# Performance work log

Measured on AMD Instinct MI355X. Metric: run time of the kernel, lower is better.

The kernel has to match this reference:

```python
import jax, jax.numpy as jnp
import numpy as np

B, D, C = 8192, 2048, 1000

def setup_inputs() -> dict:
    key = jax.random.key(0)
    k1, k2, k3 = jax.random.split(key, 3)
    x = jax.random.normal(k1, (B, D), dtype=jnp.float32)
    W = jax.random.normal(k2, (D, C), dtype=jnp.float32) * (1.0 / np.sqrt(D))
    b = jax.random.normal(k3, (C,), dtype=jnp.float32) * 0.01
    return {"x": x, "W": W, "b": b}

def reference(x, W, b):
    # inner classifier: logits out[b, c]
    out = jnp.dot(x, W) + b  # [B, C]
    # leave-one-out logsumexp per class, fused:
    # lse_k = logsumexp(out[:, != k]) = lse_all + log1p(-exp(out_k - lse_all))
    lse = jax.nn.logsumexp(out, axis=1, keepdims=True)  # [B, 1]
    loo = lse + jnp.log1p(-jnp.exp(out - lse))           # [B, C]
    # c_out = -loo; return c_out + out
    return out - loo
```

## Files before the change

### kernel.cpp

```cpp
#include <hip/hip_runtime.h>
#include <hip/hip_bf16.h>
#include <math.h>

#define BDIM 8192
#define DDIM 2048
#define CDIM 1000
#define NPAD 1024
#define BK   64

#define WS_BT_OFFSET  33554432ULL
#define WS_P0_OFFSET  37748736ULL
#define WS_P1_OFFSET  54132736ULL
#define WS_NEED       70516736ULL

typedef __attribute__((ext_vector_type(8))) short short8;
typedef __attribute__((ext_vector_type(4))) float floatx4;

__device__ __forceinline__ unsigned short f2bf(float f) {
    union { float f; unsigned u; } a; a.f = f;
    unsigned u = a.u;
    u = (u + 0x7fff + ((u >> 16) & 1)) >> 16;
    return (unsigned short)u;
}

__device__ __forceinline__ float bf2f(unsigned short h) {
    union { unsigned u; float f; } a; a.u = ((unsigned)h) << 16;
    return a.f;
}

__device__ __forceinline__ void async_copy16(const void* gp, void* lp) {
    __builtin_amdgcn_global_load_lds(
        (const __attribute__((address_space(1))) void*)gp,
        (__attribute__((address_space(3))) void*)lp,
        16, 0, 0);
}

__global__ __launch_bounds__(256) void cvt_kernel(
    const float* __restrict__ x, unsigned short* __restrict__ xb,
    const float* __restrict__ W, unsigned short* __restrict__ Bt)
{
    const int blk = blockIdx.x;
    const int t   = threadIdx.x;
    if (blk < 16384) {
        int i = blk * 256 + t;
        float4 v = ((const float4*)x)[i];
        ushort4 o;
        o.x = f2bf(v.x); o.y = f2bf(v.y); o.z = f2bf(v.z); o.w = f2bf(v.w);
        ((ushort4*)xb)[i] = o;
    } else {
        __shared__ float tile[32][33];
        const int b2 = blk - 16384;
        const int k0 = (b2 & 63) * 32;
        const int n0 = (b2 >> 6) * 32;
        const int tx = t & 31, ty = t >> 5;
        #pragma unroll
        for (int i = 0; i < 4; i++) {
            int k = k0 + ty + i * 8;
            int n = n0 + tx;
            tile[ty + i * 8][tx] = (n < CDIM) ? W[(size_t)k * CDIM + n] : 0.0f;
        }
        __syncthreads();
        #pragma unroll
        for (int i = 0; i < 4; i++) {
            int n = n0 + ty + i * 8;
            int k = k0 + tx;
            Bt[(size_t)n * DDIM + k] = f2bf(tile[tx][ty + i * 8]);
        }
    }
}

template <bool BF16OUT>
__device__ __forceinline__ void gemm_body(
    const unsigned short* __restrict__ A,
    const unsigned short* __restrict__ Bt,
    void* __restrict__ Cv,
    int mBase, int nBase, int kBase, int kIters,
    unsigned short* As, unsigned short* Bs)
{
    const int t    = threadIdx.x;
    const int wave = t >> 6;
    const int lane = t & 63;
    const int wm   = wave & 1;
    const int wn   = wave >> 1;
    const int quad = lane >> 4;
    const int l16  = lane & 15;

    floatx4 acc[4][4] = {};

    const int rowA = t >> 3;
    const int csw  = ((t & 7) ^ (rowA & 7)) * 16;
    const char* Ag = (const char*)A  + ((size_t)(mBase + rowA) * DDIM + kBase) * 2 + csw;
    const char* Bg = (const char*)Bt + ((size_t)(nBase + rowA) * DDIM + kBase) * 2 + csw;
    char* AsDst = (char*)As + t * 16;
    char* BsDst = (char*)Bs + t * 16;

    const int xorb0 = ((0 * 4 + quad) ^ (l16 & 7)) * 8;
    const int xorb1 = ((1 * 4 + quad) ^ (l16 & 7)) * 8;

    for (int kt = 0; kt < kIters * BK; kt += BK) {
        const char* a = Ag + kt * 2;
        const char* b = Bg + kt * 2;
        #pragma unroll
        for (int r = 0; r < 4; r++) {
            async_copy16(a + (size_t)r * 32 * DDIM * 2, AsDst + r * 4096);
            async_copy16(b + (size_t)r * 32 * DDIM * 2, BsDst + r * 4096);
        }
        __syncthreads();

        #pragma unroll
        for (int ks = 0; ks < 2; ks++) {
            const int xorb = ks ? xorb1 : xorb0;
            short8 af[4], bfr[4];
            #pragma unroll
            for (int mi = 0; mi < 4; mi++)
                af[mi] = *(const short8*)(As + (wm * 64 + mi * 16 + l16) * BK + xorb);
            #pragma unroll
            for (int ni = 0; ni < 4; ni++)
                bfr[ni] = *(const short8*)(Bs + (wn * 64 + ni * 16 + l16) * BK + xorb);
            #pragma unroll
            for (int mi = 0; mi < 4; mi++)
                #pragma unroll
                for (int ni = 0; ni < 4; ni++)
                    acc[mi][ni] = __builtin_amdgcn_mfma_f32_16x16x32_bf16(
                        af[mi], bfr[ni], acc[mi][ni], 0, 0, 0);
        }
        __syncthreads();
    }

    #pragma unroll
    for (int mi = 0; mi < 4; mi++) {
        int row0 = mBase + wm * 64 + mi * 16 + quad * 4;
        #pragma unroll
        for (int ni = 0; ni < 4; ni++) {
            int col = nBase + wn * 64 + ni * 16 + l16;
            if (col < CDIM) {
                #pragma unroll
                for (int rg = 0; rg < 4; rg++) {
                    if (BF16OUT)
                        ((unsigned short*)Cv)[(size_t)(row0 + rg) * CDIM + col] =
                            f2bf(acc[mi][ni][rg]);
                    else
                        ((float*)Cv)[(size_t)(row0 + rg) * CDIM + col] = acc[mi][ni][rg];
                }
            }
        }
    }
}

__global__ __launch_bounds__(256, 2) void gemm_single_kernel(
    const unsigned short* __restrict__ A,
    const unsigned short* __restrict__ Bt,
    float* __restrict__ C0)
{
    __shared__ unsigned short As[128 * BK];
    __shared__ unsigned short Bs[128 * BK];

    const int L   = blockIdx.x;
    const int xcd = L & 7;
    const int s   = L >> 3;
    const int m_t = xcd * 8 + (s >> 3);
    const int n_t = s & 7;

    gemm_body<false>(A, Bt, C0, m_t * 128, n_t * 128, 0, DDIM / BK, As, Bs);
}


#define HBUF (256 * BK)

#define STAGE_A2(BASE, EXT, KO)                                               \
    do {                                                                      \
        _Pragma("unroll")                                                     \
        for (int h = 0; h < 2; h++) {                                         \
            const int row_ = rA0 + (EXT) + h * 128;                           \
            async_copy16(gA + (size_t)row_ * DDIM + (KO),                     \
                         (BASE) + row_ * BK + c8);                            \
        }                                                                     \
    } while (0)

#define STAGE_B2(BASE, EXT, KO)                                               \
    do {                                                                      \
        _Pragma("unroll")                                                     \
        for (int h = 0; h < 2; h++) {                                         \
            const int row_ = rB0 + (EXT) + h * 128;                           \
            async_copy16(gB + (size_t)row_ * DDIM + (KO),                     \
                         (BASE) + row_ * BK + c8);                            \
        }                                                                     \
    } while (0)

#define LOADA_(BASE, MQ)                                                      \
    do {                                                                      \
        _Pragma("unroll")                                                     \
        for (int mf = 0; mf < 4; mf++) {                                      \
            const int r_ = (arA + (MQ) * 64 + mf * 16) * BK;                  \
            af[mf][0] = *(const short8*)((BASE) + r_ + xorb0);                \
            af[mf][1] = *(const short8*)((BASE) + r_ + xorb1);                \
        }                                                                     \
    } while (0)

#define LOADB_(BASE, NQ, BF)                                                  \
    do {                                                                      \
        _Pragma("unroll")                                                     \
        for (int nf = 0; nf < 2; nf++) {                                      \
            const int r_ = (arB + (NQ) * 32 + nf * 16) * BK;                  \
            BF[nf][0] = *(const short8*)((BASE) + r_ + xorb0);                \
            BF[nf][1] = *(const short8*)((BASE) + r_ + xorb1);                \
        }                                                                     \
    } while (0)

#define MMAC(MQ, NQ, BF)                                                      \
    do {                                                                      \
        __builtin_amdgcn_s_setprio(1);                                        \
        _Pragma("unroll")                                                     \
        for (int mf = 0; mf < 4; mf++) {                                      \
            _Pragma("unroll")                                                 \
            for (int nf = 0; nf < 2; nf++) {                                  \
                floatx4 c_ = acc[(MQ) * 4 + mf][(NQ) * 2 + nf];               \
                c_ = __builtin_amdgcn_mfma_f32_16x16x32_bf16(                 \
                    af[mf][0], BF[nf][0], c_, 0, 0, 0);                       \
                c_ = __builtin_amdgcn_mfma_f32_16x16x32_bf16(                 \
                    af[mf][1], BF[nf][1], c_, 0, 0, 0);                       \
                acc[(MQ) * 4 + mf][(NQ) * 2 + nf] = c_;                       \
            }                                                                 \
        }                                                                     \
        __builtin_amdgcn_s_setprio(0);                                        \
    } while (0)

#define RAW_BARRIER() asm volatile("s_barrier" ::: "memory")
#define WAIT_VM(N)    asm volatile("s_waitcnt vmcnt(" #N ")" ::: "memory")
#define WAIT_LGKM0()  asm volatile("s_waitcnt lgkmcnt(0)" ::: "memory")

__global__ __launch_bounds__(512) void gemm8_kernel(
    const unsigned short* __restrict__ A,
    const unsigned short* __restrict__ Bt,
    unsigned short* __restrict__ P0, unsigned short* __restrict__ P1)
{
    __shared__ unsigned short As[2 * HBUF];
    __shared__ unsigned short Bs[2 * HBUF];

    const int t    = threadIdx.x;
    const int wave = t >> 6;
    const int lane = t & 63;
    const int wm   = wave >> 2;
    const int wn   = wave & 3;
    const int quad = lane >> 4;
    const int l16  = lane & 15;

    const int L    = blockIdx.x;
    const int g    = (L & 7) * 32 + (L >> 3);
    const int z    = g & 1;
    const int tid2 = g >> 1;
    const int mBase = (tid2 >> 2) * 256;
    const int nBase = (tid2 & 3) * 256;
    const int kBase = z * (DDIM / 2);
    const int NTt   = (DDIM / 2) / BK;

    const int c8  = (t & 7) << 3;
    const int q0  = t >> 3;
    const int csw = (((t & 7) ^ (q0 & 7)) << 3);
    const int rA0 = q0;
    const int rB0 = q0 + (q0 & 32);
    const unsigned short* gA = A  + (size_t)mBase * DDIM + kBase + csw;
    const unsigned short* gB = Bt + (size_t)nBase * DDIM + kBase + csw;

    const int xorb0 = ((0 * 4 + quad) ^ (l16 & 7)) << 3;
    const int xorb1 = ((1 * 4 + quad) ^ (l16 & 7)) << 3;
    const int arA = wm * 128 + l16;
    const int arB = wn * 64 + l16;

    floatx4 acc[8][4] = {};
    short8 af[4][2], bf0[2][2], bf1[2][2];

    STAGE_A2(As, 0, 0);
    STAGE_A2(As, 64, 0);
    STAGE_B2(Bs, 0, 0);
    STAGE_B2(Bs, 32, 0);
    STAGE_A2(As + HBUF, 0, BK);
    STAGE_A2(As + HBUF, 64, BK);
    STAGE_B2(Bs + HBUF, 0, BK);
    STAGE_B2(Bs + HBUF, 32, BK);
    WAIT_VM(8);
    RAW_BARRIER();
    LOADA_(As, 0);
    LOADB_(Bs, 0, bf0);
    WAIT_LGKM0();
    RAW_BARRIER();

    for (int j = 0; j < NTt; j++) {
        const int bo = (j & 1) * HBUF;
        unsigned short* const cA = (unsigned short*)As + bo;
        unsigned short* const cB = (unsigned short*)Bs + bo;
        const unsigned short* const nA = (const unsigned short*)As + (bo ^ HBUF);
        const unsigned short* const nB = (const unsigned short*)Bs + (bo ^ HBUF);
        const int  ko2 = (j + 2) * BK;
        const bool s2  = (j + 2 < NTt);

        if (s2) STAGE_A2(cA, 0, ko2);
        MMAC(0, 0, bf0);
        LOADB_(cB, 1, bf1);
        RAW_BARRIER();

        if (s2) STAGE_B2(cB, 0, ko2);
        MMAC(0, 1, bf1);
        LOADA_(cA, 1);
        RAW_BARRIER();

        if (s2) STAGE_B2(cB, 32, ko2);
        MMAC(1, 0, bf0);
        if (j < NTt - 2) WAIT_VM(6);
        else             WAIT_VM(0);
        RAW_BARRIER();

        if (s2) STAGE_A2(cA, 64, ko2);
        MMAC(1, 1, bf1);
        if (j + 1 < NTt) { LOADA_(nA, 0); LOADB_(nB, 0, bf0); }
        WAIT_LGKM0();
        RAW_BARRIER();
    }

    unsigned short* P = z ? P1 : P0;
    #pragma unroll
    for (int mfg = 0; mfg < 8; mfg++) {
        const int row0 = mBase + wm * 128 + mfg * 16 + quad * 4;
        #pragma unroll
        for (int nfg = 0; nfg < 4; nfg++) {
            const int col = nBase + wn * 64 + nfg * 16 + l16;
            if (col < CDIM) {
                #pragma unroll
                for (int rg = 0; rg < 4; rg++)
                    P[(size_t)(row0 + rg) * CDIM + col] = f2bf(acc[mfg][nfg][rg]);
            }
        }
    }
}

__global__ __launch_bounds__(256) void lse_kernel(
    float* __restrict__ out,
    const unsigned short* P0, const unsigned short* P1,
    const float* __restrict__ bias, int split)
{
    const int row = blockIdx.x;
    const int t   = threadIdx.x;
    __shared__ float red[8];

    const bool valid = t < (CDIM / 4);
    const int c0 = t * 4;

    float4 v = make_float4(-INFINITY, -INFINITY, -INFINITY, -INFINITY);
    float4 e = make_float4(0.f, 0.f, 0.f, 0.f);
    if (valid) {
        if (split) {
            ushort4 p0 = *(const ushort4*)(P0 + (size_t)row * CDIM + c0);
            ushort4 p1 = *(const ushort4*)(P1 + (size_t)row * CDIM + c0);
            v.x = bf2f(p0.x) + bf2f(p1.x);
            v.y = bf2f(p0.y) + bf2f(p1.y);
            v.z = bf2f(p0.z) + bf2f(p1.z);
            v.w = bf2f(p0.w) + bf2f(p1.w);
        } else {
            v = *(const float4*)(out + (size_t)row * CDIM + c0);
        }
        float4 bb = *(const float4*)(bias + c0);
        v.x += bb.x; v.y += bb.y; v.z += bb.z; v.w += bb.w;
    }

    float m = fmaxf(fmaxf(v.x, v.y), fmaxf(v.z, v.w));
    #pragma unroll
    for (int off = 32; off > 0; off >>= 1)
        m = fmaxf(m, __shfl_down(m, off, 64));
    const int wave = t >> 6;
    if ((t & 63) == 0) red[wave] = m;
    __syncthreads();
    if (t == 0) red[4] = fmaxf(fmaxf(red[0], red[1]), fmaxf(red[2], red[3]));
    __syncthreads();
    const float M = red[4];

    float s = 0.f;
    if (valid) {
        e.x = expf(v.x - M); e.y = expf(v.y - M);
        e.z = expf(v.z - M); e.w = expf(v.w - M);
        s = e.x + e.y + e.z + e.w;
    }
    #pragma unroll
    for (int off = 32; off > 0; off >>= 1)
        s += __shfl_down(s, off, 64);
    if ((t & 63) == 0) red[wave] = s;
    __syncthreads();
    if (t == 0) red[4] = red[0] + red[1] + red[2] + red[3];
    __syncthreads();
    const float S    = red[4];
    const float lse  = M + logf(S);
    const float invS = 1.0f / S;

    if (valid) {
        float4 o;
        o.x = (v.x - lse) - log1pf(-e.x * invS);
        o.y = (v.y - lse) - log1pf(-e.y * invS);
        o.z = (v.z - lse) - log1pf(-e.z * invS);
        o.w = (v.w - lse) - log1pf(-e.w * invS);
        *(float4*)(out + (size_t)row * CDIM + c0) = o;
    }
}

extern "C" void kernel_launch(void* const* d_in, const int* in_sizes, int n_in,
                              void* d_out, int out_size, void* d_ws, size_t ws_size,
                              hipStream_t stream) {
    const float* x = (const float*)d_in[0];
    const float* W = (const float*)d_in[1];
    const float* b = (const float*)d_in[2];
    float* out = (float*)d_out;

    unsigned short* xb = (unsigned short*)d_ws;
    unsigned short* Bt = (unsigned short*)((char*)d_ws + WS_BT_OFFSET);
    unsigned short* P0 = (unsigned short*)((char*)d_ws + WS_P0_OFFSET);
    unsigned short* P1 = (unsigned short*)((char*)d_ws + WS_P1_OFFSET);
    const bool splitk = ws_size >= WS_NEED;

    cvt_kernel<<<18432, 256, 0, stream>>>(x, xb, W, Bt);

    if (splitk) {
        gemm8_kernel<<<256, 512, 0, stream>>>(xb, Bt, P0, P1);
        lse_kernel<<<BDIM, 256, 0, stream>>>(out, P0, P1, b, 1);
    } else {
        gemm_single_kernel<<<512, 256, 0, stream>>>(xb, Bt, out);
        lse_kernel<<<BDIM, 256, 0, stream>>>(out, nullptr, nullptr, b, 0);
    }
}
```

Baseline: 175.6 us.

## Fuse fp32-to-bf16 conversion of x into GEMM A-tile loading

New measurement: 185.8 us. 5.8% more time.

```diff
diff --git a/kernel.cpp b/kernel.cpp
--- a/kernel.cpp
+++ b/kernel.cpp
@@ -5,13 +5,10 @@
 #define BDIM 8192
 #define DDIM 2048
 #define CDIM 1000
-#define NPAD 1024
 #define BK   64
 
-#define WS_BT_OFFSET  33554432ULL
-#define WS_P0_OFFSET  37748736ULL
-#define WS_P1_OFFSET  54132736ULL
-#define WS_NEED       70516736ULL
+#define WS_P0_OFFSET  4194304ULL
+#define WS_P1_OFFSET  20578304ULL
 
 typedef __attribute__((ext_vector_type(8))) short short8;
 typedef __attribute__((ext_vector_type(4))) float floatx4;
@@ -35,147 +32,32 @@
         16, 0, 0);
 }
 
-__global__ __launch_bounds__(256) void cvt_kernel(
-    const float* __restrict__ x, unsigned short* __restrict__ xb,
+__global__ __launch_bounds__(256) void cvt_w_kernel(
     const float* __restrict__ W, unsigned short* __restrict__ Bt)
 {
-    const int blk = blockIdx.x;
-    const int t   = threadIdx.x;
-    if (blk < 16384) {
-        int i = blk * 256 + t;
-        float4 v = ((const float4*)x)[i];
-        ushort4 o;
-        o.x = f2bf(v.x); o.y = f2bf(v.y); o.z = f2bf(v.z); o.w = f2bf(v.w);
-        ((ushort4*)xb)[i] = o;
-    } else {
-        __shared__ float tile[32][33];
-        const int b2 = blk - 16384;
-        const int k0 = (b2 & 63) * 32;
-        const int n0 = (b2 >> 6) * 32;
-        const int tx = t & 31, ty = t >> 5;
-        #pragma unroll
-        for (int i = 0; i < 4; i++) {
-            int k = k0 + ty + i * 8;
-            int n = n0 + tx;
-            tile[ty + i * 8][tx] = (n < CDIM) ? W[(size_t)k * CDIM + n] : 0.0f;
-        }
-        __syncthreads();
-        #pragma unroll
-        for (int i = 0; i < 4; i++) {
-            int n = n0 + ty + i * 8;
-            int k = k0 + tx;
-            Bt[(size_t)n * DDIM + k] = f2bf(tile[tx][ty + i * 8]);
-        }
-    }
-}
-
-template <bool BF16OUT>
-__device__ __forceinline__ void gemm_body(
-    const unsigned short* __restrict__ A,
-    const unsigned short* __restrict__ Bt,
-    void* __restrict__ Cv,
-    int mBase, int nBase, int kBase, int kIters,
-    unsigned short* As, unsigned short* Bs)
-{
-    const int t    = threadIdx.x;
-    const int wave = t >> 6;
-    const int lane = t & 63;
-    const int wm   = wave & 1;
-    const int wn   = wave >> 1;
-    const int quad = lane >> 4;
-    const int l16  = lane & 15;
-
-    floatx4 acc[4][4] = {};
-
-    const int rowA = t >> 3;
-    const int csw  = ((t & 7) ^ (rowA & 7)) * 16;
-    const char* Ag = (const char*)A  + ((size_t)(mBase + rowA) * DDIM + kBase) * 2 + csw;
-    const char* Bg = (const char*)Bt + ((size_t)(nBase + rowA) * DDIM + kBase) * 2 + csw;
-    char* AsDst = (char*)As + t * 16;
-    char* BsDst = (char*)Bs + t * 16;
-
-    const int xorb0 = ((0 * 4 + quad) ^ (l16 & 7)) * 8;
-    const int xorb1 = ((1 * 4 + quad) ^ (l16 & 7)) * 8;
-
-    for (int kt = 0; kt < kIters * BK; kt += BK) {
-        const char* a = Ag + kt * 2;
-        const char* b = Bg + kt * 2;
-        #pragma unroll
-        for (int r = 0; r < 4; r++) {
-            async_copy16(a + (size_t)r * 32 * DDIM * 2, AsDst + r * 4096);
-            async_copy16(b + (size_t)r * 32 * DDIM * 2, BsDst + r * 4096);
-        }
-        __syncthreads();
-
-        #pragma unroll
-        for (int ks = 0; ks < 2; ks++) {
-            const int xorb = ks ? xorb1 : xorb0;
-            short8 af[4], bfr[4];
-            #pragma unroll
-            for (int mi = 0; mi < 4; mi++)
-                af[mi] = *(const short8*)(As + (wm * 64 + mi * 16 + l16) * BK + xorb);
-            #pragma unroll
-            for (int ni = 0; ni < 4; ni++)
-                bfr[ni] = *(const short8*)(Bs + (wn * 64 + ni * 16 + l16) * BK + xorb);
-            #pragma unroll
-            for (int mi = 0; mi < 4; mi++)
-                #pragma unroll
-                for (int ni = 0; ni < 4; ni++)
-                    acc[mi][ni] = __builtin_amdgcn_mfma_f32_16x16x32_bf16(
-                        af[mi], bfr[ni], acc[mi][ni], 0, 0, 0);
-        }
-        __syncthreads();
-    }
-
-    #pragma unroll
-    for (int mi = 0; mi < 4; mi++) {
-        int row0 = mBase + wm * 64 + mi * 16 + quad * 4;
-        #pragma unroll
-        for (int ni = 0; ni < 4; ni++) {
-            int col = nBase + wn * 64 + ni * 16 + l16;
-            if (col < CDIM) {
-                #pragma unroll
-                for (int rg = 0; rg < 4; rg++) {
-                    if (BF16OUT)
-                        ((unsigned short*)Cv)[(size_t)(row0 + rg) * CDIM + col] =
-                            f2bf(acc[mi][ni][rg]);
-                    else
-                        ((float*)Cv)[(size_t)(row0 + rg) * CDIM + col] = acc[mi][ni][rg];
-                }
-            }
-        }
-    }
-}
-
-__global__ __launch_bounds__(256, 2) void gemm_single_kernel(
-    const unsigned short* __restrict__ A,
-    const unsigned short* __restrict__ Bt,
-    float* __restrict__ C0)
-{
-    __shared__ unsigned short As[128 * BK];
-    __shared__ unsigned short Bs[128 * BK];
-
-    const int L   = blockIdx.x;
-    const int xcd = L & 7;
-    const int s   = L >> 3;
-    const int m_t = xcd * 8 + (s >> 3);
-    const int n_t = s & 7;
-
-    gemm_body<false>(A, Bt, C0, m_t * 128, n_t * 128, 0, DDIM / BK, As, Bs);
+    __shared__ float tile[32][33];
+    const int b2 = blockIdx.x;
+    const int t  = threadIdx.x;
+    const int k0 = (b2 & 63) * 32;
+    const int n0 = (b2 >> 6) * 32;
+    const int tx = t & 31, ty = t >> 5;
+    #pragma unroll
+    for (int i = 0; i < 4; i++) {
+        int k = k0 + ty + i * 8;
+        int n = n0 + tx;
+        tile[ty + i * 8][tx] = (n < CDIM) ? W[(size_t)k * CDIM + n] : 0.0f;
+    }
+    __syncthreads();
+    #pragma unroll
+    for (int i = 0; i < 4; i++) {
+        int n = n0 + ty + i * 8;
+        int k = k0 + tx;
+        Bt[(size_t)n * DDIM + k] = f2bf(tile[tx][ty + i * 8]);
+    }
 }
 
 
 #define HBUF (256 * BK)
-
-#define STAGE_A2(BASE, EXT, KO)                                               \
-    do {                                                                      \
-        _Pragma("unroll")                                                     \
-        for (int h = 0; h < 2; h++) {                                         \
-            const int row_ = rA0 + (EXT) + h * 128;                           \
-            async_copy16(gA + (size_t)row_ * DDIM + (KO),                     \
-                         (BASE) + row_ * BK + c8);                            \
-        }                                                                     \
-    } while (0)
 
 #define STAGE_B2(BASE, EXT, KO)                                               \
     do {                                                                      \
@@ -184,6 +66,32 @@
             const int row_ = rB0 + (EXT) + h * 128;                           \
             async_copy16(gB + (size_t)row_ * DDIM + (KO),                     \
                          (BASE) + row_ * BK + c8);                            \
+        }                                                                     \
+    } while (0)
+
+#define ISSUE_A(SL, EXT, KO)                                                  \
+    do {                                                                      \
+        const float* p0_ = gAf + (size_t)(q0 + (EXT)) * DDIM + (KO);          \
+        const float* p1_ = p0_ + (size_t)128 * DDIM;                          \
+        axr[(SL) + 0] = *(const float4*)(p0_);                                \
+        axr[(SL) + 1] = *(const float4*)(p0_ + 4);                            \
+        axr[(SL) + 2] = *(const float4*)(p1_);                                \
+        axr[(SL) + 3] = *(const float4*)(p1_ + 4);                            \
+    } while (0)
+
+#define WRITE_A(BASE, SL, EXT)                                                \
+    do {                                                                      \
+        _Pragma("unroll")                                                     \
+        for (int r_ = 0; r_ < 2; r_++) {                                      \
+            const int row_ = q0 + (EXT) + r_ * 128;                           \
+            float4 lo_ = axr[(SL) + r_ * 2];                                  \
+            float4 hi_ = axr[(SL) + r_ * 2 + 1];                              \
+            short8 pk_;                                                       \
+            pk_[0] = (short)f2bf(lo_.x); pk_[1] = (short)f2bf(lo_.y);         \
+            pk_[2] = (short)f2bf(lo_.z); pk_[3] = (short)f2bf(lo_.w);         \
+            pk_[4] = (short)f2bf(hi_.x); pk_[5] = (short)f2bf(hi_.y);         \
+            pk_[6] = (short)f2bf(hi_.z); pk_[7] = (short)f2bf(hi_.w);         \
+            *(short8*)((BASE) + row_ * BK + csw) = pk_;                       \
         }                                                                     \
     } while (0)
 
@@ -230,7 +138,7 @@
 #define WAIT_LGKM0()  asm volatile("s_waitcnt lgkmcnt(0)" ::: "memory")
 
 __global__ __launch_bounds__(512) void gemm8_kernel(
-    const unsigned short* __restrict__ A,
+    const float* __restrict__ X,
     const unsigned short* __restrict__ Bt,
     unsigned short* __restrict__ P0, unsigned short* __restrict__ P1)
 {
@@ -257,9 +165,8 @@
     const int c8  = (t & 7) << 3;
     const int q0  = t >> 3;
     const int csw = (((t & 7) ^ (q0 & 7)) << 3);
-    const int rA0 = q0;
     const int rB0 = q0 + (q0 & 32);
-    const unsigned short* gA = A  + (size_t)mBase * DDIM + kBase + csw;
+    const float* gAf = X + (size_t)mBase * DDIM + kBase + ((t & 7) << 3);
     const unsigned short* gB = Bt + (size_t)nBase * DDIM + kBase + csw;
 
     const int xorb0 = ((0 * 4 + quad) ^ (l16 & 7)) << 3;
@@ -269,16 +176,23 @@
 
     floatx4 acc[8][4] = {};
     short8 af[4][2], bf0[2][2], bf1[2][2];
-
-    STAGE_A2(As, 0, 0);
-    STAGE_A2(As, 64, 0);
+    float4 axr[8];
+
+    ISSUE_A(0, 0, 0);
+    ISSUE_A(4, 64, 0);
+    WAIT_VM(0);
+    WRITE_A(As, 0, 0);
+    WRITE_A(As, 4, 64);
     STAGE_B2(Bs, 0, 0);
     STAGE_B2(Bs, 32, 0);
-    STAGE_A2(As + HBUF, 0, BK);
-    STAGE_A2(As + HBUF, 64, BK);
+    ISSUE_A(0, 0, BK);
+    ISSUE_A(4, 64, BK);
+    WAIT_VM(0);
+    WRITE_A(As + HBUF, 0, 0);
+    WRITE_A(As + HBUF, 4, 64);
     STAGE_B2(Bs + HBUF, 0, BK);
     STAGE_B2(Bs + HBUF, 32, BK);
-    WAIT_VM(8);
+    WAIT_LGKM0();
     RAW_BARRIER();
     LOADA_(As, 0);
     LOADB_(Bs, 0, bf0);
@@ -294,23 +208,31 @@
         const int  ko2 = (j + 2) * BK;
         const bool s2  = (j + 2 < NTt);
 
-        if (s2) STAGE_A2(cA, 0, ko2);
+        if (s2) ISSUE_A(0, 0, ko2);
         MMAC(0, 0, bf0);
         LOADB_(cB, 1, bf1);
         RAW_BARRIER();
 
         if (s2) STAGE_B2(cB, 0, ko2);
+        if (s2) ISSUE_A(4, 64, ko2);
         MMAC(0, 1, bf1);
         LOADA_(cA, 1);
         RAW_BARRIER();
 
-        if (s2) STAGE_B2(cB, 32, ko2);
+        if (s2) {
+            STAGE_B2(cB, 32, ko2);
+            WAIT_VM(8);
+            WRITE_A(cA, 0, 0);
+        }
         MMAC(1, 0, bf0);
-        if (j < NTt - 2) WAIT_VM(6);
-        else             WAIT_VM(0);
         RAW_BARRIER();
 
-        if (s2) STAGE_A2(cA, 64, ko2);
+        if (s2) {
+            WAIT_VM(4);
+            WRITE_A(cA, 4, 64);
+        } else {
+            WAIT_VM(0);
+        }
         MMAC(1, 1, bf1);
         if (j + 1 < NTt) { LOADA_(nA, 0); LOADB_(nB, 0, bf0); }
         WAIT_LGKM0();
@@ -408,19 +330,13 @@
     const float* b = (const float*)d_in[2];
     float* out = (float*)d_out;
 
-    unsigned short* xb = (unsigned short*)d_ws;
-    unsigned short* Bt = (unsigned short*)((char*)d_ws + WS_BT_OFFSET);
+    unsigned short* Bt = (unsigned short*)d_ws;
     unsigned short* P0 = (unsigned short*)((char*)d_ws + WS_P0_OFFSET);
     unsigned short* P1 = (unsigned short*)((char*)d_ws + WS_P1_OFFSET);
-    const bool splitk = ws_size >= WS_NEED;
-
-    cvt_kernel<<<18432, 256, 0, stream>>>(x, xb, W, Bt);
-
-    if (splitk) {
-        gemm8_kernel<<<256, 512, 0, stream>>>(xb, Bt, P0, P1);
-        lse_kernel<<<BDIM, 256, 0, stream>>>(out, P0, P1, b, 1);
-    } else {
-        gemm_single_kernel<<<512, 256, 0, stream>>>(xb, Bt, out);
-        lse_kernel<<<BDIM, 256, 0, stream>>>(out, nullptr, nullptr, b, 0);
-    }
-}
+
+    cvt_w_kernel<<<2048, 256, 0, stream>>>(W, Bt);
+
+    gemm8_kernel<<<256, 512, 0, stream>>>(x, Bt, P0, P1);
+
+    lse_kernel<<<BDIM, 256, 0, stream>>>(out, P0, P1, b, 1);
+}
```
